# Kernel tuning notes

Hardware: AMD Instinct MI355X
Metric: run time of the kernel (lower is better)

The kernel has to match this reference:

```python
import jax, jax.numpy as jnp
import numpy as np

B, C, N = 2, 4, 200000
M = N // 8  # bytes in the bitmask per (b, c)


def _quat_to_rotmat(quats):
    # quats: (..., 4) -> R: (..., 3, 3)
    q = quats * jax.lax.rsqrt(jnp.sum(quats * quats, -1, keepdims=True))
    w, x, y, z = q[..., 0], q[..., 1], q[..., 2], q[..., 3]
    R = jnp.stack([
        1 - 2 * (y * y + z * z), 2 * (x * y - w * z), 2 * (x * z + w * y),
        2 * (x * y + w * z), 1 - 2 * (x * x + z * z), 2 * (y * z - w * x),
        2 * (x * z - w * y), 2 * (y * z + w * x), 1 - 2 * (x * x + y * y)], -1)
    return R.reshape(q.shape[:-1] + (3, 3))


def _quat_to_rotmat_vjp(quats, v_R):
    inv_norm = jax.lax.rsqrt(jnp.sum(quats * quats, -1, keepdims=True))
    qn = quats * inv_norm
    w, x, y, z = qn[..., 0], qn[..., 1], qn[..., 2], qn[..., 3]
    a = v_R[..., 2, 1] - v_R[..., 1, 2]
    b = v_R[..., 0, 2] - v_R[..., 2, 0]
    c = v_R[..., 1, 0] - v_R[..., 0, 1]
    s11_22 = v_R[..., 1, 1] + v_R[..., 2, 2]
    s00_22 = v_R[..., 0, 0] + v_R[..., 2, 2]
    s00_11 = v_R[..., 0, 0] + v_R[..., 1, 1]
    p01 = v_R[..., 1, 0] + v_R[..., 0, 1]
    p02 = v_R[..., 2, 0] + v_R[..., 0, 2]
    p12 = v_R[..., 2, 1] + v_R[..., 1, 2]
    v_qn = jnp.stack([
        2.0 * (x * a + y * b + z * c),
        2.0 * (-2.0 * x * s11_22 + y * p01 + z * p02 + w * a),
        2.0 * (x * p01 - 2.0 * y * s00_22 + z * p12 + w * b),
        2.0 * (x * p02 + y * p12 - 2.0 * z * s00_11 + w * c)], -1)
    return (v_qn - jnp.sum(v_qn * qn, -1, keepdims=True) * qn) * inv_norm


def _forward(means, quats, scales, conics, viewmats, Ks, v_means2d, v_depths,
             v_conics, v_colors_culling, v_opacities_culling, filter_mask,
             width, height):
    means = jnp.transpose(means, (0, 2, 1))            # (B,N,3)
    quats = jnp.transpose(quats, (0, 2, 1))            # (B,N,4)
    scales = jnp.transpose(scales, (0, 2, 1))          # (B,N,3)
    conics = jnp.transpose(conics, (0, 1, 3, 2))       # (B,C,N,3)
    v_m2d = jnp.transpose(v_means2d, (0, 1, 3, 2))     # (B,C,N,2)
    v_con = jnp.transpose(v_conics, (0, 1, 3, 2))      # (B,C,N,3)
    v_col = jnp.transpose(v_colors_culling, (0, 1, 3, 2))  # (B,C,N,3)
    v_op = v_opacities_culling                          # (B,C,N)
    v_dep = v_depths                                    # (B,C,N)
    Bv, Cv, Nv = v_op.shape

    # unpack uint8 bitmask (LSB first), decompact culled grads back to N slots
    bits = ((filter_mask[..., None] >> jnp.arange(8, dtype=filter_mask.dtype)) & 1) != 0
    fb = bits.reshape(Bv, Cv, -1)[:, :, :Nv]            # (B,C,N) bool
    rank = jnp.clip(jnp.cumsum(fb.astype(jnp.int32), axis=-1) - 1, 0, Nv - 1)

    def decompact(v):
        if v.ndim == 3:
            return jnp.where(fb, jnp.take_along_axis(v, rank, axis=2), 0.0)
        return jnp.where(fb[..., None], jnp.take_along_axis(v, rank[..., None], axis=2), 0.0)

    v_con_o = decompact(v_con)
    v_m2d_o = decompact(v_m2d)
    v_dep_o = decompact(v_dep)
    v_col_o = decompact(v_col)
    v_op_o = decompact(v_op)

    # conic (inverse 2x2 covariance) VJP
    covar2d_inv = jnp.stack([conics[..., 0], conics[..., 1], conics[..., 1], conics[..., 2]], -1)
    covar2d_inv = covar2d_inv.reshape(conics.shape[:-1] + (2, 2))
    v_ci = jnp.stack([v_con_o[..., 0], v_con_o[..., 1] * 0.5, v_con_o[..., 1] * 0.5, v_con_o[..., 2]], -1)
    v_ci = v_ci.reshape(conics.shape[:-1] + (2, 2))
    v_covar2d = -covar2d_inv @ v_ci @ covar2d_inv        # (B,C,N,2,2)

    Rv = viewmats[..., :3, :3]                           # (B,C,3,3)
    t = viewmats[..., :3, 3]                             # (B,C,3)
    rotmat = _quat_to_rotmat(quats)                      # (B,N,3,3)
    Mm = rotmat * scales[..., None, :]
    covars = jnp.einsum('bnij,bnkj->bnik', Mm, Mm)       # (B,N,3,3)
    mean_c = jnp.einsum('bcij,bnj->bcni', Rv, means) + t[..., None, :]  # (B,C,N,3)
    covar_c = jnp.einsum('bcij,bnjk,bclk->bcnil', Rv, covars, Rv)       # (B,C,N,3,3)

    # perspective projection VJP
    mx, my, tz = mean_c[..., 0], mean_c[..., 1], mean_c[..., 2]
    tz2 = tz * tz
    tz3 = tz2 * tz
    fx = Ks[..., 0, 0, None]
    fy = Ks[..., 1, 1, None]
    cx = Ks[..., 0, 2, None]
    cy = Ks[..., 1, 2, None]
    tan_fovx = 0.5 * width / fx
    tan_fovy = 0.5 * height / fy
    lim_x_pos = (width - cx) / fx + 0.3 * tan_fovx
    lim_x_neg = cx / fx + 0.3 * tan_fovx
    lim_y_pos = (height - cy) / fy + 0.3 * tan_fovy
    lim_y_neg = cy / fy + 0.3 * tan_fovy
    xf = ((mx / tz <= lim_x_pos) & (mx / tz >= -lim_x_neg)).astype(tz.dtype)
    yf = ((my / tz <= lim_y_pos) & (my / tz >= -lim_y_neg)).astype(tz.dtype)
    tx = tz * jnp.clip(mx / tz, -lim_x_neg, lim_x_pos)
    ty = tz * jnp.clip(my / tz, -lim_y_neg, lim_y_pos)
    O = jnp.zeros_like(tz)
    J = jnp.stack([fx / tz, O, -fx * tx / tz2, O, fy / tz, -fy * ty / tz2], -1)
    J = J.reshape(tz.shape + (2, 3))                     # (B,C,N,2,3)
    v_cov3d = jnp.swapaxes(J, -2, -1) @ v_covar2d @ J    # (B,C,N,3,3)
    vm0, vm1 = v_m2d_o[..., 0], v_m2d_o[..., 1]
    m0 = fx / tz * vm0
    m1 = fy / tz * vm1
    m2 = -(fx * mx * vm0 + fy * my * vm1) / tz2
    v_J = v_covar2d @ J @ jnp.swapaxes(covar_c, -2, -1) + jnp.swapaxes(v_covar2d, -2, -1) @ J @ covar_c
    vJ00, vJ02 = v_J[..., 0, 0], v_J[..., 0, 2]
    vJ11, vJ12 = v_J[..., 1, 1], v_J[..., 1, 2]
    m0 = m0 - fx / tz2 * vJ02 * xf
    m2 = m2 - fx / tz3 * vJ02 * tx * (1.0 - xf)
    m1 = m1 - fy / tz2 * vJ12 * yf
    m2 = m2 - fy / tz3 * vJ12 * ty * (1.0 - yf)
    m2 = m2 - fx / tz2 * vJ00 - fy / tz2 * vJ11 + 2.0 * fx * tx / tz3 * vJ02 + 2.0 * fy * ty / tz3 * vJ12
    m2 = m2 + v_dep_o
    v_mean_c = jnp.stack([m0, m1, m2], -1)               # (B,C,N,3)

    # world-to-camera VJPs
    v_Rview = jnp.einsum('bcni,bnj->bcij', v_mean_c, means)
    v_pW = jnp.einsum('bcji,bcnj->bni', Rv, v_mean_c)
    v_Rview = v_Rview + jnp.einsum('bcnij,bcjk,bnlk->bcil', v_cov3d, Rv, covars) \
                      + jnp.einsum('bcnji,bcjk,bnkl->bcil', v_cov3d, Rv, covars)
    v_covarW = jnp.einsum('bcij,bcnik,bckl->bnjl', Rv, v_cov3d, Rv)

    # quat/scale -> covariance VJP
    v_M = (v_covarW + jnp.swapaxes(v_covarW, -2, -1)) @ Mm
    v_Rrot = v_M * scales[..., None, :]
    v_quats = _quat_to_rotmat_vjp(quats, v_Rrot)         # (B,N,4)
    v_scales = jnp.einsum('bnij,bnij->bnj', rotmat, v_M) # (B,N,3)

    v_colors_final = jnp.transpose(v_col_o.sum(axis=1), (0, 2, 1))  # (B,3,N)
    v_opacities_final = v_op_o.sum(axis=1)               # (B,N)
    return (v_pW, v_quats, v_scales, v_Rview, v_colors_final, v_opacities_final)


def setup_inputs() -> dict:
    key = jax.random.key(0)
    k = jax.random.split(key, 12)
    means = jax.random.normal(k[0], (B, 3, N), jnp.float32)
    quats = jax.random.normal(k[1], (B, 4, N), jnp.float32)
    scales = 0.1 + 0.4 * jax.random.uniform(k[2], (B, 3, N), dtype=jnp.float32)
    conics = 0.1 * jax.random.normal(k[3], (B, C, 3, N), jnp.float32)
    viewmats = jnp.tile(jnp.eye(4, dtype=jnp.float32), (B, C, 1, 1)) \
             + 0.05 * jax.random.normal(k[4], (B, C, 4, 4), jnp.float32)
    viewmats = viewmats.at[..., 2, 3].add(5.0)  # keep tz away from 0
    Kmat = jnp.array([[500.0, 0.0, 324.0], [0.0, 500.0, 210.0], [0.0, 0.0, 1.0]], jnp.float32)
    Ks = jnp.tile(Kmat, (B, C, 1, 1))
    v_means2d = 0.05 * jax.random.normal(k[5], (B, C, 2, N), jnp.float32)
    v_depths = 0.05 * jax.random.normal(k[6], (B, C, N), jnp.float32)
    v_conics = 0.05 * jax.random.normal(k[7], (B, C, 3, N), jnp.float32)
    v_colors_culling = 0.05 * jax.random.normal(k[8], (B, C, 3, N), jnp.float32)
    v_opacities_culling = 0.05 * jax.random.normal(k[9], (B, C, N), jnp.float32)
    filter_mask = jax.random.randint(k[10], (B, C, M), 0, 256, jnp.int32)
    return {"means": means, "quats": quats, "scales": scales, "conics": conics,
            "viewmats": viewmats, "Ks": Ks, "v_means2d": v_means2d,
            "v_depths": v_depths, "v_conics": v_conics,
            "v_colors_culling": v_colors_culling,
            "v_opacities_culling": v_opacities_culling,
            "filter_mask": filter_mask, "width": 648, "height": 420}


def reference(means, quats, scales, conics, viewmats, Ks, v_means2d, v_depths,
              v_conics, v_colors_culling, v_opacities_culling, filter_mask,
              width, height):
    return _forward(means, quats, scales, conics, viewmats, Ks, v_means2d,
                    v_depths, v_conics, v_colors_culling, v_opacities_culling,
                    filter_mask, width, height)
```

## Files before the change

kernel.cpp:

```cpp
#include <hip/hip_runtime.h>

#define NPTS 200000
#define MWORDS 25000
#define NCHUNK 98
#define NSLOT 64

#define WS_PREFIX    0
#define WS_BLOCKSUM  800000
#define WS_CHUNKPREF 803136
#define WS_SLOTS     806272
#define WS_CAM       824704

__global__ __launch_bounds__(256) void scan1_kernel(const int* __restrict__ mask,
                                                    int* __restrict__ prefix,
                                                    int* __restrict__ blocksum) {
    const int bc    = blockIdx.y;
    const int chunk = blockIdx.x;
    const int tid   = threadIdx.x;
    const int lane  = tid & 63, wv = tid >> 6;
    const int w = chunk * 256 + tid;
    const int base = bc * MWORDS;

    int p = (w < MWORDS) ? __popc(mask[base + w]) : 0;
    int v = p;
#pragma unroll
    for (int off = 1; off < 64; off <<= 1) {
        int u = __shfl_up(v, off, 64);
        if (lane >= off) v += u;
    }
    __shared__ int wsum[4];
    if (lane == 63) wsum[wv] = v;
    __syncthreads();
    int wadd = 0;
#pragma unroll
    for (int i = 0; i < 4; i++) if (i < wv) wadd += wsum[i];
    int excl = v - p + wadd;
    if (w < MWORDS) prefix[base + w] = excl;
    if (tid == 255) blocksum[bc * NCHUNK + chunk] = wadd + v;
}

__global__ __launch_bounds__(1024) void scan2_kernel(const int* __restrict__ blocksum,
                                                     int* __restrict__ chunkpref,
                                                     float* __restrict__ slots,
                                                     float* __restrict__ cam,
                                                     const float* __restrict__ viewmats,
                                                     const float* __restrict__ Ks,
                                                     const int* __restrict__ pw,
                                                     const int* __restrict__ ph) {
    const int tid = threadIdx.x;
    __shared__ int s[8 * NCHUNK];
    if (tid < 8 * NCHUNK) s[tid] = blocksum[tid];
    __syncthreads();
    if (tid < 8) {
        int running = 0;
        for (int j = 0; j < NCHUNK; j++) {
            int idx = tid * NCHUNK + j;
            int t = s[idx];
            s[idx] = running;
            running += t;
        }
    }
    __syncthreads();
    if (tid < 8 * NCHUNK) chunkpref[tid] = s[tid];

    for (int i = tid; i < NSLOT * 72; i += 1024) slots[i] = 0.f;

    if (tid < 8) {
        const int bc = tid;
        float* cp = cam + bc * 20;
        const int vbase = bc * 16;
        for (int i = 0; i < 3; i++) {
            for (int j = 0; j < 3; j++) cp[i*3 + j] = viewmats[vbase + i*4 + j];
            cp[9 + i] = viewmats[vbase + i*4 + 3];
        }
        const int kbase = bc * 9;
        float fx = Ks[kbase + 0], fy = Ks[kbase + 4];
        float cx = Ks[kbase + 2], cy = Ks[kbase + 5];
        int wi = *pw, hi = *ph;
        float W = (wi >= 1 && wi <= (1 << 20)) ? (float)wi : __int_as_float(wi);
        float H = (hi >= 1 && hi <= (1 << 20)) ? (float)hi : __int_as_float(hi);
        float tanx = 0.5f * W / fx, tany = 0.5f * H / fy;
        cp[12] = fx; cp[13] = fy;
        cp[14] = (W - cx) / fx + 0.3f * tanx;
        cp[15] = cx / fx + 0.3f * tanx;
        cp[16] = (H - cy) / fy + 0.3f * tany;
        cp[17] = cy / fy + 0.3f * tany;
    }
}

__global__ __launch_bounds__(256) void main_kernel(
    const float* __restrict__ means,
    const float* __restrict__ quats,
    const float* __restrict__ scales,
    const float* __restrict__ conics,
    const float* __restrict__ v_m2d,
    const float* __restrict__ v_dep,
    const float* __restrict__ v_con,
    const float* __restrict__ v_col,
    const float* __restrict__ v_op,
    const int* __restrict__ mask,
    const int* __restrict__ prefix,
    const int* __restrict__ chunkpref,
    const float* __restrict__ cam,
    float* __restrict__ slots,
    float* __restrict__ out)
{
    const int O_PW = 0, O_QU = 1200000, O_SC = 2800000, O_CL = 4000072, O_OP = 5200072;
    const int b = blockIdx.y;
    const int n = blockIdx.x * 256 + threadIdx.x;
    const bool act = (n < NPTS);

    float rv[4][9];
#pragma unroll
    for (int c = 0; c < 4; c++)
#pragma unroll
        for (int k = 0; k < 9; k++) rv[c][k] = 0.f;

    float H00=0,H01=0,H02=0,H11=0,H12=0,H22=0;
    float vpw0=0,vpw1=0,vpw2=0;
    float vcl0=0,vcl1=0,vcl2=0, vopo=0;
    float qw=0,qx=0,qy=0,qz=0, inv_norm=1.f;
    float R00=0,R01=0,R02=0,R10=0,R11=0,R12=0,R20=0,R21=0,R22=0;
    float M00=0,M01=0,M02=0,M10=0,M11=0,M12=0,M20=0,M21=0,M22=0;
    float cv00=0,cv01=0,cv02=0,cv11=0,cv12=0,cv22=0;
    float mn0=0,mn1=0,mn2=0, sc0=0,sc1=0,sc2=0;

    if (act) {
        const int w_ = n >> 3, bit = n & 7, chk = w_ >> 8;
        int words[4], pref[4];
#pragma unroll
        for (int c = 0; c < 4; c++) {
            const int bc = b*4 + c;
            words[c] = mask[bc*MWORDS + w_];
            pref[c]  = prefix[bc*MWORDS + w_] + chunkpref[bc*NCHUNK + chk];
        }

        mn0 = means[(b*3+0)*NPTS + n];
        mn1 = means[(b*3+1)*NPTS + n];
        mn2 = means[(b*3+2)*NPTS + n];
        float q0 = quats[(b*4+0)*NPTS + n];
        float q1 = quats[(b*4+1)*NPTS + n];
        float q2 = quats[(b*4+2)*NPTS + n];
        float q3 = quats[(b*4+3)*NPTS + n];
        sc0 = scales[(b*3+0)*NPTS + n];
        sc1 = scales[(b*3+1)*NPTS + n];
        sc2 = scales[(b*3+2)*NPTS + n];
        inv_norm = rsqrtf(q0*q0 + q1*q1 + q2*q2 + q3*q3);
        qw = q0*inv_norm; qx = q1*inv_norm; qy = q2*inv_norm; qz = q3*inv_norm;
        R00 = 1.f - 2.f*(qy*qy + qz*qz); R01 = 2.f*(qx*qy - qw*qz); R02 = 2.f*(qx*qz + qw*qy);
        R10 = 2.f*(qx*qy + qw*qz); R11 = 1.f - 2.f*(qx*qx + qz*qz); R12 = 2.f*(qy*qz - qw*qx);
        R20 = 2.f*(qx*qz - qw*qy); R21 = 2.f*(qy*qz + qw*qx); R22 = 1.f - 2.f*(qx*qx + qy*qy);
        M00 = R00*sc0; M01 = R01*sc1; M02 = R02*sc2;
        M10 = R10*sc0; M11 = R11*sc1; M12 = R12*sc2;
        M20 = R20*sc0; M21 = R21*sc1; M22 = R22*sc2;
        cv00 = M00*M00 + M01*M01 + M02*M02;
        cv01 = M00*M10 + M01*M11 + M02*M12;
        cv02 = M00*M20 + M01*M21 + M02*M22;
        cv11 = M10*M10 + M11*M11 + M12*M12;
        cv12 = M10*M20 + M11*M21 + M12*M22;
        cv22 = M20*M20 + M21*M21 + M22*M22;

#pragma unroll
        for (int c = 0; c < 4; c++) {
            const int bc = b*4 + c;
            const float* cp = cam + bc*20;
            const float V00=cp[0],V01=cp[1],V02=cp[2],V10=cp[3],V11=cp[4],V12=cp[5],V20=cp[6],V21=cp[7],V22=cp[8];
            const float t0=cp[9], t1=cp[10], t2=cp[11];
            const float fx=cp[12], fy=cp[13], lxp=cp[14], lxn=cp[15], lyp=cp[16], lyn=cp[17];
            const int word = words[c];
            if ((word >> bit) & 1) {
                const int r = pref[c] + __popc(word & ((1 << bit) - 1));
                const int base3 = bc*3*NPTS, base2 = bc*2*NPTS, base1 = bc*NPTS;
                float g_c0 = v_con[base3 + r];
                float g_c1 = v_con[base3 + NPTS + r];
                float g_c2 = v_con[base3 + 2*NPTS + r];
                float g_m0 = v_m2d[base2 + r];
                float g_m1 = v_m2d[base2 + NPTS + r];
                float g_d  = v_dep[base1 + r];
                float g_l0 = v_col[base3 + r];
                float g_l1 = v_col[base3 + NPTS + r];
                float g_l2 = v_col[base3 + 2*NPTS + r];
                float g_o  = v_op[base1 + r];
                float p00 = conics[base3 + n];
                float p01 = conics[base3 + NPTS + n];
                float p11 = conics[base3 + 2*NPTS + n];
                float a00 = g_c0, a01 = 0.5f*g_c1, a11 = g_c2;
                float q00 = a00*p00 + a01*p01, q01 = a00*p01 + a01*p11;
                float q10 = a01*p00 + a11*p01, q11 = a01*p01 + a11*p11;
                float u00 = -(p00*q00 + p01*q10), u01 = -(p00*q01 + p01*q11);
                float u10 = -(p01*q00 + p11*q10), u11 = -(p01*q01 + p11*q11);
                float mx = V00*mn0 + V01*mn1 + V02*mn2 + t0;
                float my = V10*mn0 + V11*mn1 + V12*mn2 + t1;
                float tz = V20*mn0 + V21*mn1 + V22*mn2 + t2;
                float rz = 1.0f / tz;
                float rz2 = rz*rz, rz3 = rz2*rz;
                float T00 = V00*cv00 + V01*cv01 + V02*cv02;
                float T01 = V00*cv01 + V01*cv11 + V02*cv12;
                float T02 = V00*cv02 + V01*cv12 + V02*cv22;
                float T10 = V10*cv00 + V11*cv01 + V12*cv02;
                float T11 = V10*cv01 + V11*cv11 + V12*cv12;
                float T12 = V10*cv02 + V11*cv12 + V12*cv22;
                float T20 = V20*cv00 + V21*cv01 + V22*cv02;
                float T21 = V20*cv01 + V21*cv11 + V22*cv12;
                float T22 = V20*cv02 + V21*cv12 + V22*cv22;
                float cc00 = T00*V00 + T01*V01 + T02*V02;
                float cc01 = T00*V10 + T01*V11 + T02*V12;
                float cc02 = T00*V20 + T01*V21 + T02*V22;
                float cc11 = T10*V10 + T11*V11 + T12*V12;
                float cc12 = T10*V20 + T11*V21 + T12*V22;
                float cc22 = T20*V20 + T21*V21 + T22*V22;
                float mxz = mx*rz, myz = my*rz;
                float xf = (mxz <= lxp && mxz >= -lxn) ? 1.f : 0.f;
                float yf = (myz <= lyp && myz >= -lyn) ? 1.f : 0.f;
                float tx = tz * fminf(fmaxf(mxz, -lxn), lxp);
                float ty = tz * fminf(fmaxf(myz, -lyn), lyp);
                float j00 = fx*rz, j02 = -fx*tx*rz2;
                float j11 = fy*rz, j12 = -fy*ty*rz2;
                float W0a = u00*j00, W0b = u01*j11, W0c = u00*j02 + u01*j12;
                float W1a = u10*j00, W1b = u11*j11, W1c = u10*j02 + u11*j12;
                float d00 = j00*W0a, d01 = j00*W0b, d02 = j00*W0c;
                float d10 = j11*W1a, d11 = j11*W1b, d12 = j11*W1c;
                float d20 = j02*W0a + j12*W1a, d21 = j02*W0b + j12*W1b, d22 = j02*W0c + j12*W1c;
                float s00 = d00+d00, s01 = d01+d10, s02 = d02+d20;
                float s11 = d11+d11, s12 = d12+d21, s22 = d22+d22;
                float e00 = u00+u00, e01 = u01+u10, e11 = u11+u11;
                float X00 = e00*j00, X01 = e01*j11, X02 = e00*j02 + e01*j12;
                float X10 = e01*j00, X11 = e11*j11, X12 = e01*j02 + e11*j12;
                float vJ00 = X00*cc00 + X01*cc01 + X02*cc02;
                float vJ02 = X00*cc02 + X01*cc12 + X02*cc22;
                float vJ11 = X10*cc01 + X11*cc11 + X12*cc12;
                float vJ12 = X10*cc02 + X11*cc12 + X12*cc22;
                float m0 = fx*rz*g_m0;
                float m1 = fy*rz*g_m1;
                float m2 = -(fx*mx*g_m0 + fy*my*g_m1)*rz2;
                m0 -= fx*rz2*vJ02*xf;
                m2 -= fx*rz3*vJ02*tx*(1.f - xf);
                m1 -= fy*rz2*vJ12*yf;
                m2 -= fy*rz3*vJ12*ty*(1.f - yf);
                m2 += -fx*rz2*vJ00 - fy*rz2*vJ11 + 2.f*fx*tx*rz3*vJ02 + 2.f*fy*ty*rz3*vJ12;
                m2 += g_d;
                vpw0 += V00*m0 + V10*m1 + V20*m2;
                vpw1 += V01*m0 + V11*m1 + V21*m2;
                vpw2 += V02*m0 + V12*m1 + V22*m2;
                rv[c][0] += m0*mn0 + (s00*T00 + s01*T10 + s02*T20);
                rv[c][1] += m0*mn1 + (s00*T01 + s01*T11 + s02*T21);
                rv[c][2] += m0*mn2 + (s00*T02 + s01*T12 + s02*T22);
                rv[c][3] += m1*mn0 + (s01*T00 + s11*T10 + s12*T20);
                rv[c][4] += m1*mn1 + (s01*T01 + s11*T11 + s12*T21);
                rv[c][5] += m1*mn2 + (s01*T02 + s11*T12 + s12*T22);
                rv[c][6] += m2*mn0 + (s02*T00 + s12*T10 + s22*T20);
                rv[c][7] += m2*mn1 + (s02*T01 + s12*T11 + s22*T21);
                rv[c][8] += m2*mn2 + (s02*T02 + s12*T12 + s22*T22);
                float P00 = s00*V00 + s01*V10 + s02*V20;
                float P01 = s00*V01 + s01*V11 + s02*V21;
                float P02 = s00*V02 + s01*V12 + s02*V22;
                float P10 = s01*V00 + s11*V10 + s12*V20;
                float P11 = s01*V01 + s11*V11 + s12*V21;
                float P12 = s01*V02 + s11*V12 + s12*V22;
                float P20 = s02*V00 + s12*V10 + s22*V20;
                float P21 = s02*V01 + s12*V11 + s22*V21;
                float P22 = s02*V02 + s12*V12 + s22*V22;
                H00 += V00*P00 + V10*P10 + V20*P20;
                H01 += V00*P01 + V10*P11 + V20*P21;
                H02 += V00*P02 + V10*P12 + V20*P22;
                H11 += V01*P01 + V11*P11 + V21*P21;
                H12 += V01*P02 + V11*P12 + V21*P22;
                H22 += V02*P02 + V12*P12 + V22*P22;
                vcl0 += g_l0; vcl1 += g_l1; vcl2 += g_l2; vopo += g_o;
            }
        }
    }

#pragma unroll
    for (int off = 32; off >= 1; off >>= 1) {
#pragma unroll
        for (int c = 0; c < 4; c++)
#pragma unroll
            for (int k = 0; k < 9; k++)
                rv[c][k] += __shfl_down(rv[c][k], off, 64);
    }
    __shared__ float redbuf[4][36];
    const int lane = threadIdx.x & 63, wv = threadIdx.x >> 6;
    if (lane == 0) {
#pragma unroll
        for (int c = 0; c < 4; c++)
#pragma unroll
            for (int k = 0; k < 9; k++) redbuf[wv][c*9 + k] = rv[c][k];
    }
    __syncthreads();
    if (threadIdx.x < 36) {
        float s = redbuf[0][threadIdx.x] + redbuf[1][threadIdx.x] +
                  redbuf[2][threadIdx.x] + redbuf[3][threadIdx.x];
        const int slot = blockIdx.x & (NSLOT - 1);
        atomicAdd(&slots[slot*72 + b*36 + threadIdx.x], s);
    }

    if (act) {
        float vM00 = H00*M00 + H01*M10 + H02*M20;
        float vM01 = H00*M01 + H01*M11 + H02*M21;
        float vM02 = H00*M02 + H01*M12 + H02*M22;
        float vM10 = H01*M00 + H11*M10 + H12*M20;
        float vM11 = H01*M01 + H11*M11 + H12*M21;
        float vM12 = H01*M02 + H11*M12 + H12*M22;
        float vM20 = H02*M00 + H12*M10 + H22*M20;
        float vM21 = H02*M01 + H12*M11 + H22*M21;
        float vM22 = H02*M02 + H12*M12 + H22*M22;
        float vs0 = R00*vM00 + R10*vM10 + R20*vM20;
        float vs1 = R01*vM01 + R11*vM11 + R21*vM21;
        float vs2 = R02*vM02 + R12*vM12 + R22*vM22;
        float G00 = vM00*sc0, G01 = vM01*sc1, G02 = vM02*sc2;
        float G10 = vM10*sc0, G11 = vM11*sc1, G12 = vM12*sc2;
        float G20 = vM20*sc0, G21 = vM21*sc1, G22 = vM22*sc2;
        float a_ = G21 - G12, b_ = G02 - G20, c_ = G10 - G01;
        float s1122 = G11 + G22, s0022 = G00 + G22, s0011 = G00 + G11;
        float pp01 = G10 + G01, pp02 = G20 + G02, pp12 = G21 + G12;
        float vq0 = 2.f*(qx*a_ + qy*b_ + qz*c_);
        float vq1 = 2.f*(-2.f*qx*s1122 + qy*pp01 + qz*pp02 + qw*a_);
        float vq2 = 2.f*(qx*pp01 - 2.f*qy*s0022 + qz*pp12 + qw*b_);
        float vq3 = 2.f*(qx*pp02 + qy*pp12 - 2.f*qz*s0011 + qw*c_);
        float dot = vq0*qw + vq1*qx + vq2*qy + vq3*qz;
        float o0 = (vq0 - dot*qw)*inv_norm;
        float o1 = (vq1 - dot*qx)*inv_norm;
        float o2 = (vq2 - dot*qy)*inv_norm;
        float o3 = (vq3 - dot*qz)*inv_norm;

        const int pwb = b*NPTS + n;
        out[O_PW + pwb*3 + 0] = vpw0;
        out[O_PW + pwb*3 + 1] = vpw1;
        out[O_PW + pwb*3 + 2] = vpw2;
        float4 qv = make_float4(o0, o1, o2, o3);
        *reinterpret_cast<float4*>(out + O_QU + pwb*4) = qv;
        out[O_SC + pwb*3 + 0] = vs0;
        out[O_SC + pwb*3 + 1] = vs1;
        out[O_SC + pwb*3 + 2] = vs2;
        out[O_CL + (b*3+0)*NPTS + n] = vcl0;
        out[O_CL + (b*3+1)*NPTS + n] = vcl1;
        out[O_CL + (b*3+2)*NPTS + n] = vcl2;
        out[O_OP + b*NPTS + n] = vopo;
    }
}

__global__ void fin_kernel(const float* __restrict__ slots, float* __restrict__ out) {
    int t = threadIdx.x;
    if (t < 72) {
        float s = 0.f;
#pragma unroll
        for (int i = 0; i < NSLOT; i++) s += slots[i*72 + t];
        out[4000000 + t] = s;
    }
}

extern "C" void kernel_launch(void* const* d_in, const int* in_sizes, int n_in,
                              void* d_out, int out_size, void* d_ws, size_t ws_size,
                              hipStream_t stream) {
    (void)in_sizes; (void)n_in; (void)out_size; (void)ws_size;
    const float* means    = (const float*)d_in[0];
    const float* quats    = (const float*)d_in[1];
    const float* scales   = (const float*)d_in[2];
    const float* conics   = (const float*)d_in[3];
    const float* viewmats = (const float*)d_in[4];
    const float* Ks       = (const float*)d_in[5];
    const float* v_m2d    = (const float*)d_in[6];
    const float* v_dep    = (const float*)d_in[7];
    const float* v_con    = (const float*)d_in[8];
    const float* v_col    = (const float*)d_in[9];
    const float* v_op     = (const float*)d_in[10];
    const int* mask = (const int*)d_in[11];
    const int* pw   = (const int*)d_in[12];
    const int* ph   = (const int*)d_in[13];
    float* out = (float*)d_out;

    char* ws = (char*)d_ws;
    int*   prefix    = (int*)(ws + WS_PREFIX);
    int*   blocksum  = (int*)(ws + WS_BLOCKSUM);
    int*   chunkpref = (int*)(ws + WS_CHUNKPREF);
    float* slots     = (float*)(ws + WS_SLOTS);
    float* cam       = (float*)(ws + WS_CAM);

    scan1_kernel<<<dim3(NCHUNK, 8), dim3(256), 0, stream>>>(mask, prefix, blocksum);
    scan2_kernel<<<dim3(1), dim3(1024), 0, stream>>>(blocksum, chunkpref, slots, cam,
                                                     viewmats, Ks, pw, ph);
    main_kernel<<<dim3((NPTS + 255) / 256, 2), dim3(256), 0, stream>>>(
        means, quats, scales, conics, v_m2d, v_dep, v_con, v_col, v_op,
        mask, prefix, chunkpref, cam, slots, out);
    fin_kernel<<<dim3(1), dim3(128), 0, stream>>>(slots, out);
}
```

Before: 169.1 us.

## Remove scan2 kernel, compute chunk prefix in main kernel, use DPP reductions

Drops the single-block scan2 launch: camera setup and slot zeroing move into an extra block of scan1, and each main-kernel block derives its chunk prefix itself by summing the preceding block sums with a wave reduction. The per-camera rotation-gradient accumulators now go through DPP wave reductions, with per-wave atomics replacing the 36-register array, shuffle tree and LDS block reduction. Inactive threads clamp their index instead of branching. The aim is to save one kernel launch and serial scan latency, plus register pressure, at the cost of redundant block-sum reads and more atomics per block.

```diff
diff --git a/kernel.cpp b/kernel.cpp
--- a/kernel.cpp
+++ b/kernel.cpp
@@ -7,16 +7,66 @@
 
 #define WS_PREFIX    0
 #define WS_BLOCKSUM  800000
-#define WS_CHUNKPREF 803136
-#define WS_SLOTS     806272
-#define WS_CAM       824704
+#define WS_SLOTS     803136
+#define WS_CAM       821568
+
+__device__ __forceinline__ float wred_f(float x) {
+    x += __int_as_float(__builtin_amdgcn_update_dpp(0, __float_as_int(x), 0x111, 0xf, 0xf, true));
+    x += __int_as_float(__builtin_amdgcn_update_dpp(0, __float_as_int(x), 0x112, 0xf, 0xf, true));
+    x += __int_as_float(__builtin_amdgcn_update_dpp(0, __float_as_int(x), 0x114, 0xf, 0xf, true));
+    x += __int_as_float(__builtin_amdgcn_update_dpp(0, __float_as_int(x), 0x118, 0xf, 0xf, true));
+    x += __int_as_float(__builtin_amdgcn_update_dpp(0, __float_as_int(x), 0x142, 0xf, 0xf, true));
+    x += __int_as_float(__builtin_amdgcn_update_dpp(0, __float_as_int(x), 0x143, 0xf, 0xf, true));
+    return x;
+}
+__device__ __forceinline__ int wred_i(int x) {
+    x += __builtin_amdgcn_update_dpp(0, x, 0x111, 0xf, 0xf, true);
+    x += __builtin_amdgcn_update_dpp(0, x, 0x112, 0xf, 0xf, true);
+    x += __builtin_amdgcn_update_dpp(0, x, 0x114, 0xf, 0xf, true);
+    x += __builtin_amdgcn_update_dpp(0, x, 0x118, 0xf, 0xf, true);
+    x += __builtin_amdgcn_update_dpp(0, x, 0x142, 0xf, 0xf, true);
+    x += __builtin_amdgcn_update_dpp(0, x, 0x143, 0xf, 0xf, true);
+    return x;
+}
 
 __global__ __launch_bounds__(256) void scan1_kernel(const int* __restrict__ mask,
                                                     int* __restrict__ prefix,
-                                                    int* __restrict__ blocksum) {
+                                                    int* __restrict__ blocksum,
+                                                    float* __restrict__ slots,
+                                                    float* __restrict__ cam,
+                                                    const float* __restrict__ viewmats,
+                                                    const float* __restrict__ Ks,
+                                                    const int* __restrict__ pw,
+                                                    const int* __restrict__ ph) {
+    const int tid = threadIdx.x;
+    if (blockIdx.x == NCHUNK) {
+        if (blockIdx.y != 0) return;
+        for (int i = tid; i < NSLOT * 72; i += 256) slots[i] = 0.f;
+        if (tid < 8) {
+            const int bc = tid;
+            float* cp = cam + bc * 20;
+            const int vbase = bc * 16;
+            for (int i = 0; i < 3; i++) {
+                for (int j = 0; j < 3; j++) cp[i*3 + j] = viewmats[vbase + i*4 + j];
+                cp[9 + i] = viewmats[vbase + i*4 + 3];
+            }
+            const int kbase = bc * 9;
+            float fx = Ks[kbase + 0], fy = Ks[kbase + 4];
+            float cx = Ks[kbase + 2], cy = Ks[kbase + 5];
+            int wi = *pw, hi = *ph;
+            float W = (wi >= 1 && wi <= (1 << 20)) ? (float)wi : __int_as_float(wi);
+            float H = (hi >= 1 && hi <= (1 << 20)) ? (float)hi : __int_as_float(hi);
+            float tanx = 0.5f * W / fx, tany = 0.5f * H / fy;
+            cp[12] = fx; cp[13] = fy;
+            cp[14] = (W - cx) / fx + 0.3f * tanx;
+            cp[15] = cx / fx + 0.3f * tanx;
+            cp[16] = (H - cy) / fy + 0.3f * tany;
+            cp[17] = cy / fy + 0.3f * tany;
+        }
+        return;
+    }
     const int bc    = blockIdx.y;
     const int chunk = blockIdx.x;
-    const int tid   = threadIdx.x;
     const int lane  = tid & 63, wv = tid >> 6;
     const int w = chunk * 256 + tid;
     const int base = bc * MWORDS;
@@ -34,58 +84,8 @@
     int wadd = 0;
 #pragma unroll
     for (int i = 0; i < 4; i++) if (i < wv) wadd += wsum[i];
-    int excl = v - p + wadd;
-    if (w < MWORDS) prefix[base + w] = excl;
+    if (w < MWORDS) prefix[base + w] = v - p + wadd;
     if (tid == 255) blocksum[bc * NCHUNK + chunk] = wadd + v;
-}
-
-__global__ __launch_bounds__(1024) void scan2_kernel(const int* __restrict__ blocksum,
-                                                     int* __restrict__ chunkpref,
-                                                     float* __restrict__ slots,
-                                                     float* __restrict__ cam,
-                                                     const float* __restrict__ viewmats,
-                                                     const float* __restrict__ Ks,
-                                                     const int* __restrict__ pw,
-                                                     const int* __restrict__ ph) {
-    const int tid = threadIdx.x;
-    __shared__ int s[8 * NCHUNK];
-    if (tid < 8 * NCHUNK) s[tid] = blocksum[tid];
-    __syncthreads();
-    if (tid < 8) {
-        int running = 0;
-        for (int j = 0; j < NCHUNK; j++) {
-            int idx = tid * NCHUNK + j;
-            int t = s[idx];
-            s[idx] = running;
-            running += t;
-        }
-    }
-    __syncthreads();
-    if (tid < 8 * NCHUNK) chunkpref[tid] = s[tid];
-
-    for (int i = tid; i < NSLOT * 72; i += 1024) slots[i] = 0.f;
-
-    if (tid < 8) {
-        const int bc = tid;
-        float* cp = cam + bc * 20;
-        const int vbase = bc * 16;
-        for (int i = 0; i < 3; i++) {
-            for (int j = 0; j < 3; j++) cp[i*3 + j] = viewmats[vbase + i*4 + j];
-            cp[9 + i] = viewmats[vbase + i*4 + 3];
-        }
-        const int kbase = bc * 9;
-        float fx = Ks[kbase + 0], fy = Ks[kbase + 4];
-        float cx = Ks[kbase + 2], cy = Ks[kbase + 5];
-        int wi = *pw, hi = *ph;
-        float W = (wi >= 1 && wi <= (1 << 20)) ? (float)wi : __int_as_float(wi);
-        float H = (hi >= 1 && hi <= (1 << 20)) ? (float)hi : __int_as_float(hi);
-        float tanx = 0.5f * W / fx, tany = 0.5f * H / fy;
-        cp[12] = fx; cp[13] = fy;
-        cp[14] = (W - cx) / fx + 0.3f * tanx;
-        cp[15] = cx / fx + 0.3f * tanx;
-        cp[16] = (H - cy) / fy + 0.3f * tany;
-        cp[17] = cy / fy + 0.3f * tany;
-    }
 }
 
 __global__ __launch_bounds__(256) void main_kernel(
@@ -100,7 +100,7 @@
     const float* __restrict__ v_op,
     const int* __restrict__ mask,
     const int* __restrict__ prefix,
-    const int* __restrict__ chunkpref,
+    const int* __restrict__ blocksum,
     const float* __restrict__ cam,
     float* __restrict__ slots,
     float* __restrict__ out)
@@ -109,190 +109,179 @@
     const int b = blockIdx.y;
     const int n = blockIdx.x * 256 + threadIdx.x;
     const bool act = (n < NPTS);
-
-    float rv[4][9];
-#pragma unroll
-    for (int c = 0; c < 4; c++)
-#pragma unroll
-        for (int k = 0; k < 9; k++) rv[c][k] = 0.f;
+    const int nc = act ? n : (NPTS - 1);
+    const int lane = threadIdx.x & 63, wv = threadIdx.x >> 6;
+    const int slot = blockIdx.x & (NSLOT - 1);
+
+    const int chk = blockIdx.x >> 3;
+    __shared__ int cpf_lds[4];
+    {
+        const int bcw = b * 4 + wv;
+        int s0 = (lane < chk) ? blocksum[bcw * NCHUNK + lane] : 0;
+        if (lane + 64 < chk) s0 += blocksum[bcw * NCHUNK + lane + 64];
+        int tot = wred_i(s0);
+        int t = __builtin_amdgcn_readlane(tot, 63);
+        if (lane == 0) cpf_lds[wv] = t;
+    }
+
+    const int w_ = nc >> 3, bit = nc & 7;
+    int words[4], pref[4];
+#pragma unroll
+    for (int c = 0; c < 4; c++) {
+        const int bc = b*4 + c;
+        words[c] = mask[bc*MWORDS + w_];
+        pref[c]  = prefix[bc*MWORDS + w_];
+    }
+
+    float mn0 = means[(b*3+0)*NPTS + nc];
+    float mn1 = means[(b*3+1)*NPTS + nc];
+    float mn2 = means[(b*3+2)*NPTS + nc];
+    float q0 = quats[(b*4+0)*NPTS + nc];
+    float q1 = quats[(b*4+1)*NPTS + nc];
+    float q2 = quats[(b*4+2)*NPTS + nc];
+    float q3 = quats[(b*4+3)*NPTS + nc];
+    float sc0 = scales[(b*3+0)*NPTS + nc];
+    float sc1 = scales[(b*3+1)*NPTS + nc];
+    float sc2 = scales[(b*3+2)*NPTS + nc];
+    float inv_norm = rsqrtf(q0*q0 + q1*q1 + q2*q2 + q3*q3);
+    float qw = q0*inv_norm, qx = q1*inv_norm, qy = q2*inv_norm, qz = q3*inv_norm;
+    float R00 = 1.f - 2.f*(qy*qy + qz*qz), R01 = 2.f*(qx*qy - qw*qz), R02 = 2.f*(qx*qz + qw*qy);
+    float R10 = 2.f*(qx*qy + qw*qz), R11 = 1.f - 2.f*(qx*qx + qz*qz), R12 = 2.f*(qy*qz - qw*qx);
+    float R20 = 2.f*(qx*qz - qw*qy), R21 = 2.f*(qy*qz + qw*qx), R22 = 1.f - 2.f*(qx*qx + qy*qy);
+    float M00 = R00*sc0, M01 = R01*sc1, M02 = R02*sc2;
+    float M10 = R10*sc0, M11 = R11*sc1, M12 = R12*sc2;
+    float M20 = R20*sc0, M21 = R21*sc1, M22 = R22*sc2;
+    float cv00 = M00*M00 + M01*M01 + M02*M02;
+    float cv01 = M00*M10 + M01*M11 + M02*M12;
+    float cv02 = M00*M20 + M01*M21 + M02*M22;
+    float cv11 = M10*M10 + M11*M11 + M12*M12;
+    float cv12 = M10*M20 + M11*M21 + M12*M22;
+    float cv22 = M20*M20 + M21*M21 + M22*M22;
 
     float H00=0,H01=0,H02=0,H11=0,H12=0,H22=0;
     float vpw0=0,vpw1=0,vpw2=0;
     float vcl0=0,vcl1=0,vcl2=0, vopo=0;
-    float qw=0,qx=0,qy=0,qz=0, inv_norm=1.f;
-    float R00=0,R01=0,R02=0,R10=0,R11=0,R12=0,R20=0,R21=0,R22=0;
-    float M00=0,M01=0,M02=0,M10=0,M11=0,M12=0,M20=0,M21=0,M22=0;
-    float cv00=0,cv01=0,cv02=0,cv11=0,cv12=0,cv22=0;
-    float mn0=0,mn1=0,mn2=0, sc0=0,sc1=0,sc2=0;
-
-    if (act) {
-        const int w_ = n >> 3, bit = n & 7, chk = w_ >> 8;
-        int words[4], pref[4];
-#pragma unroll
-        for (int c = 0; c < 4; c++) {
-            const int bc = b*4 + c;
-            words[c] = mask[bc*MWORDS + w_];
-            pref[c]  = prefix[bc*MWORDS + w_] + chunkpref[bc*NCHUNK + chk];
-        }
-
-        mn0 = means[(b*3+0)*NPTS + n];
-        mn1 = means[(b*3+1)*NPTS + n];
-        mn2 = means[(b*3+2)*NPTS + n];
-        float q0 = quats[(b*4+0)*NPTS + n];
-        float q1 = quats[(b*4+1)*NPTS + n];
-        float q2 = quats[(b*4+2)*NPTS + n];
-        float q3 = quats[(b*4+3)*NPTS + n];
-        sc0 = scales[(b*3+0)*NPTS + n];
-        sc1 = scales[(b*3+1)*NPTS + n];
-        sc2 = scales[(b*3+2)*NPTS + n];
-        inv_norm = rsqrtf(q0*q0 + q1*q1 + q2*q2 + q3*q3);
-        qw = q0*inv_norm; qx = q1*inv_norm; qy = q2*inv_norm; qz = q3*inv_norm;
-        R00 = 1.f - 2.f*(qy*qy + qz*qz); R01 = 2.f*(qx*qy - qw*qz); R02 = 2.f*(qx*qz + qw*qy);
-        R10 = 2.f*(qx*qy + qw*qz); R11 = 1.f - 2.f*(qx*qx + qz*qz); R12 = 2.f*(qy*qz - qw*qx);
-        R20 = 2.f*(qx*qz - qw*qy); R21 = 2.f*(qy*qz + qw*qx); R22 = 1.f - 2.f*(qx*qx + qy*qy);
-        M00 = R00*sc0; M01 = R01*sc1; M02 = R02*sc2;
-        M10 = R10*sc0; M11 = R11*sc1; M12 = R12*sc2;
-        M20 = R20*sc0; M21 = R21*sc1; M22 = R22*sc2;
-        cv00 = M00*M00 + M01*M01 + M02*M02;
-        cv01 = M00*M10 + M01*M11 + M02*M12;
-        cv02 = M00*M20 + M01*M21 + M02*M22;
-        cv11 = M10*M10 + M11*M11 + M12*M12;
-        cv12 = M10*M20 + M11*M21 + M12*M22;
-        cv22 = M20*M20 + M21*M21 + M22*M22;
-
-#pragma unroll
-        for (int c = 0; c < 4; c++) {
-            const int bc = b*4 + c;
-            const float* cp = cam + bc*20;
+
+    __syncthreads();
+
+#pragma unroll
+    for (int c = 0; c < 4; c++) {
+        const int bc = b*4 + c;
+        const float* cp = cam + bc*20;
+        const bool go = act && ((words[c] >> bit) & 1);
+        float rv0=0,rv1=0,rv2=0,rv3=0,rv4=0,rv5=0,rv6=0,rv7=0,rv8=0;
+        if (go) {
             const float V00=cp[0],V01=cp[1],V02=cp[2],V10=cp[3],V11=cp[4],V12=cp[5],V20=cp[6],V21=cp[7],V22=cp[8];
             const float t0=cp[9], t1=cp[10], t2=cp[11];
             const float fx=cp[12], fy=cp[13], lxp=cp[14], lxn=cp[15], lyp=cp[16], lyn=cp[17];
-            const int word = words[c];
-            if ((word >> bit) & 1) {
-                const int r = pref[c] + __popc(word & ((1 << bit) - 1));
-                const int base3 = bc*3*NPTS, base2 = bc*2*NPTS, base1 = bc*NPTS;
-                float g_c0 = v_con[base3 + r];
-                float g_c1 = v_con[base3 + NPTS + r];
-                float g_c2 = v_con[base3 + 2*NPTS + r];
-                float g_m0 = v_m2d[base2 + r];
-                float g_m1 = v_m2d[base2 + NPTS + r];
-                float g_d  = v_dep[base1 + r];
-                float g_l0 = v_col[base3 + r];
-                float g_l1 = v_col[base3 + NPTS + r];
-                float g_l2 = v_col[base3 + 2*NPTS + r];
-                float g_o  = v_op[base1 + r];
-                float p00 = conics[base3 + n];
-                float p01 = conics[base3 + NPTS + n];
-                float p11 = conics[base3 + 2*NPTS + n];
-                float a00 = g_c0, a01 = 0.5f*g_c1, a11 = g_c2;
-                float q00 = a00*p00 + a01*p01, q01 = a00*p01 + a01*p11;
-                float q10 = a01*p00 + a11*p01, q11 = a01*p01 + a11*p11;
-                float u00 = -(p00*q00 + p01*q10), u01 = -(p00*q01 + p01*q11);
-                float u10 = -(p01*q00 + p11*q10), u11 = -(p01*q01 + p11*q11);
-                float mx = V00*mn0 + V01*mn1 + V02*mn2 + t0;
-                float my = V10*mn0 + V11*mn1 + V12*mn2 + t1;
-                float tz = V20*mn0 + V21*mn1 + V22*mn2 + t2;
-                float rz = 1.0f / tz;
-                float rz2 = rz*rz, rz3 = rz2*rz;
-                float T00 = V00*cv00 + V01*cv01 + V02*cv02;
-                float T01 = V00*cv01 + V01*cv11 + V02*cv12;
-                float T02 = V00*cv02 + V01*cv12 + V02*cv22;
-                float T10 = V10*cv00 + V11*cv01 + V12*cv02;
-                float T11 = V10*cv01 + V11*cv11 + V12*cv12;
-                float T12 = V10*cv02 + V11*cv12 + V12*cv22;
-                float T20 = V20*cv00 + V21*cv01 + V22*cv02;
-                float T21 = V20*cv01 + V21*cv11 + V22*cv12;
-                float T22 = V20*cv02 + V21*cv12 + V22*cv22;
-                float cc00 = T00*V00 + T01*V01 + T02*V02;
-                float cc01 = T00*V10 + T01*V11 + T02*V12;
-                float cc02 = T00*V20 + T01*V21 + T02*V22;
-                float cc11 = T10*V10 + T11*V11 + T12*V12;
-                float cc12 = T10*V20 + T11*V21 + T12*V22;
-                float cc22 = T20*V20 + T21*V21 + T22*V22;
-                float mxz = mx*rz, myz = my*rz;
-                float xf = (mxz <= lxp && mxz >= -lxn) ? 1.f : 0.f;
-                float yf = (myz <= lyp && myz >= -lyn) ? 1.f : 0.f;
-                float tx = tz * fminf(fmaxf(mxz, -lxn), lxp);
-                float ty = tz * fminf(fmaxf(myz, -lyn), lyp);
-                float j00 = fx*rz, j02 = -fx*tx*rz2;
-                float j11 = fy*rz, j12 = -fy*ty*rz2;
-                float W0a = u00*j00, W0b = u01*j11, W0c = u00*j02 + u01*j12;
-                float W1a = u10*j00, W1b = u11*j11, W1c = u10*j02 + u11*j12;
-                float d00 = j00*W0a, d01 = j00*W0b, d02 = j00*W0c;
-                float d10 = j11*W1a, d11 = j11*W1b, d12 = j11*W1c;
-                float d20 = j02*W0a + j12*W1a, d21 = j02*W0b + j12*W1b, d22 = j02*W0c + j12*W1c;
-                float s00 = d00+d00, s01 = d01+d10, s02 = d02+d20;
-                float s11 = d11+d11, s12 = d12+d21, s22 = d22+d22;
-                float e00 = u00+u00, e01 = u01+u10, e11 = u11+u11;
-                float X00 = e00*j00, X01 = e01*j11, X02 = e00*j02 + e01*j12;
-                float X10 = e01*j00, X11 = e11*j11, X12 = e01*j02 + e11*j12;
-                float vJ00 = X00*cc00 + X01*cc01 + X02*cc02;
-                float vJ02 = X00*cc02 + X01*cc12 + X02*cc22;
-                float vJ11 = X10*cc01 + X11*cc11 + X12*cc12;
-                float vJ12 = X10*cc02 + X11*cc12 + X12*cc22;
-                float m0 = fx*rz*g_m0;
-                float m1 = fy*rz*g_m1;
-                float m2 = -(fx*mx*g_m0 + fy*my*g_m1)*rz2;
-                m0 -= fx*rz2*vJ02*xf;
-                m2 -= fx*rz3*vJ02*tx*(1.f - xf);
-                m1 -= fy*rz2*vJ12*yf;
-                m2 -= fy*rz3*vJ12*ty*(1.f - yf);
-                m2 += -fx*rz2*vJ00 - fy*rz2*vJ11 + 2.f*fx*tx*rz3*vJ02 + 2.f*fy*ty*rz3*vJ12;
-                m2 += g_d;
-                vpw0 += V00*m0 + V10*m1 + V20*m2;
-                vpw1 += V01*m0 + V11*m1 + V21*m2;
-                vpw2 += V02*m0 + V12*m1 + V22*m2;
-                rv[c][0] += m0*mn0 + (s00*T00 + s01*T10 + s02*T20);
-                rv[c][1] += m0*mn1 + (s00*T01 + s01*T11 + s02*T21);
-                rv[c][2] += m0*mn2 + (s00*T02 + s01*T12 + s02*T22);
-                rv[c][3] += m1*mn0 + (s01*T00 + s11*T10 + s12*T20);
-                rv[c][4] += m1*mn1 + (s01*T01 + s11*T11 + s12*T21);
-                rv[c][5] += m1*mn2 + (s01*T02 + s11*T12 + s12*T22);
-                rv[c][6] += m2*mn0 + (s02*T00 + s12*T10 + s22*T20);
-                rv[c][7] += m2*mn1 + (s02*T01 + s12*T11 + s22*T21);
-                rv[c][8] += m2*mn2 + (s02*T02 + s12*T12 + s22*T22);
-                float P00 = s00*V00 + s01*V10 + s02*V20;
-                float P01 = s00*V01 + s01*V11 + s02*V21;
-                float P02 = s00*V02 + s01*V12 + s02*V22;
-                float P10 = s01*V00 + s11*V10 + s12*V20;
-                float P11 = s01*V01 + s11*V11 + s12*V21;
-                float P12 = s01*V02 + s11*V12 + s12*V22;
-                float P20 = s02*V00 + s12*V10 + s22*V20;
-                float P21 = s02*V01 + s12*V11 + s22*V21;
-                float P22 = s02*V02 + s12*V12 + s22*V22;
-                H00 += V00*P00 + V10*P10 + V20*P20;
-                H01 += V00*P01 + V10*P11 + V20*P21;
-                H02 += V00*P02 + V10*P12 + V20*P22;
-                H11 += V01*P01 + V11*P11 + V21*P21;
-                H12 += V01*P02 + V11*P12 + V21*P22;
-                H22 += V02*P02 + V12*P12 + V22*P22;
-                vcl0 += g_l0; vcl1 += g_l1; vcl2 += g_l2; vopo += g_o;
-            }
+            const int r = pref[c] + cpf_lds[c] + __popc(words[c] & ((1 << bit) - 1));
+            const int base3 = bc*3*NPTS, base2 = bc*2*NPTS, base1 = bc*NPTS;
+            float g_c0 = v_con[base3 + r];
+            float g_c1 = v_con[base3 + NPTS + r];
+            float g_c2 = v_con[base3 + 2*NPTS + r];
+            float g_m0 = v_m2d[base2 + r];
+            float g_m1 = v_m2d[base2 + NPTS + r];
+            float g_d  = v_dep[base1 + r];
+            float g_l0 = v_col[base3 + r];
+            float g_l1 = v_col[base3 + NPTS + r];
+            float g_l2 = v_col[base3 + 2*NPTS + r];
+            float g_o  = v_op[base1 + r];
+            float p00 = conics[base3 + nc];
+            float p01 = conics[base3 + NPTS + nc];
+            float p11 = conics[base3 + 2*NPTS + nc];
+            float a00 = g_c0, a01 = 0.5f*g_c1, a11 = g_c2;
+            float q00 = a00*p00 + a01*p01, q01 = a00*p01 + a01*p11;
+            float q10 = a01*p00 + a11*p01, q11 = a01*p01 + a11*p11;
+            float u00 = -(p00*q00 + p01*q10), u01 = -(p00*q01 + p01*q11);
+            float u10 = -(p01*q00 + p11*q10), u11 = -(p01*q01 + p11*q11);
+            float mx = V00*mn0 + V01*mn1 + V02*mn2 + t0;
+            float my = V10*mn0 + V11*mn1 + V12*mn2 + t1;
+            float tz = V20*mn0 + V21*mn1 + V22*mn2 + t2;
+            float rz = 1.0f / tz;
+            float rz2 = rz*rz, rz3 = rz2*rz;
+            float T00 = V00*cv00 + V01*cv01 + V02*cv02;
+            float T01 = V00*cv01 + V01*cv11 + V02*cv12;
+            float T02 = V00*cv02 + V01*cv12 + V02*cv22;
+            float T10 = V10*cv00 + V11*cv01 + V12*cv02;
+            float T11 = V10*cv01 + V11*cv11 + V12*cv12;
+            float T12 = V10*cv02 + V11*cv12 + V12*cv22;
+            float T20 = V20*cv00 + V21*cv01 + V22*cv02;
+            float T21 = V20*cv01 + V21*cv11 + V22*cv12;
+            float T22 = V20*cv02 + V21*cv12 + V22*cv22;
+            float cc00 = T00*V00 + T01*V01 + T02*V02;
+            float cc01 = T00*V10 + T01*V11 + T02*V12;
+            float cc02 = T00*V20 + T01*V21 + T02*V22;
+            float cc11 = T10*V10 + T11*V11 + T12*V12;
+            float cc12 = T10*V20 + T11*V21 + T12*V22;
+            float cc22 = T20*V20 + T21*V21 + T22*V22;
+            float mxz = mx*rz, myz = my*rz;
+            float xf = (mxz <= lxp && mxz >= -lxn) ? 1.f : 0.f;
+            float yf = (myz <= lyp && myz >= -lyn) ? 1.f : 0.f;
+            float tx = tz * fminf(fmaxf(mxz, -lxn), lxp);
+            float ty = tz * fminf(fmaxf(myz, -lyn), lyp);
+            float j00 = fx*rz, j02 = -fx*tx*rz2;
+            float j11 = fy*rz, j12 = -fy*ty*rz2;
+            float W0a = u00*j00, W0b = u01*j11, W0c = u00*j02 + u01*j12;
+            float W1a = u10*j00, W1b = u11*j11, W1c = u10*j02 + u11*j12;
+            float d00 = j00*W0a, d01 = j00*W0b, d02 = j00*W0c;
+            float d10 = j11*W1a, d11 = j11*W1b, d12 = j11*W1c;
+            float d20 = j02*W0a + j12*W1a, d21 = j02*W0b + j12*W1b, d22 = j02*W0c + j12*W1c;
+            float s00 = d00+d00, s01 = d01+d10, s02 = d02+d20;
+            float s11 = d11+d11, s12 = d12+d21, s22 = d22+d22;
+            float e00 = u00+u00, e01 = u01+u10, e11 = u11+u11;
+            float X00 = e00*j00, X01 = e01*j11, X02 = e00*j02 + e01*j12;
+            float X10 = e01*j00, X11 = e11*j11, X12 = e01*j02 + e11*j12;
+            float vJ00 = X00*cc00 + X01*cc01 + X02*cc02;
+            float vJ02 = X00*cc02 + X01*cc12 + X02*cc22;
+            float vJ11 = X10*cc01 + X11*cc11 + X12*cc12;
+            float vJ12 = X10*cc02 + X11*cc12 + X12*cc22;
+            float m0 = fx*rz*g_m0;
+            float m1 = fy*rz*g_m1;
+            float m2 = -(fx*mx*g_m0 + fy*my*g_m1)*rz2;
+            m0 -= fx*rz2*vJ02*xf;
+            m2 -= fx*rz3*vJ02*tx*(1.f - xf);
+            m1 -= fy*rz2*vJ12*yf;
+            m2 -= fy*rz3*vJ12*ty*(1.f - yf);
+            m2 += -fx*rz2*vJ00 - fy*rz2*vJ11 + 2.f*fx*tx*rz3*vJ02 + 2.f*fy*ty*rz3*vJ12;
+            m2 += g_d;
+            vpw0 += V00*m0 + V10*m1 + V20*m2;
+            vpw1 += V01*m0 + V11*m1 + V21*m2;
+            vpw2 += V02*m0 + V12*m1 + V22*m2;
+            rv0 = m0*mn0 + (s00*T00 + s01*T10 + s02*T20);
+            rv1 = m0*mn1 + (s00*T01 + s01*T11 + s02*T21);
+            rv2 = m0*mn2 + (s00*T02 + s01*T12 + s02*T22);
+            rv3 = m1*mn0 + (s01*T00 + s11*T10 + s12*T20);
+            rv4 = m1*mn1 + (s01*T01 + s11*T11 + s12*T21);
+            rv5 = m1*mn2 + (s01*T02 + s11*T12 + s12*T22);
+            rv6 = m2*mn0 + (s02*T00 + s12*T10 + s22*T20);
+            rv7 = m2*mn1 + (s02*T01 + s12*T11 + s22*T21);
+            rv8 = m2*mn2 + (s02*T02 + s12*T12 + s22*T22);
+            float P00 = s00*V00 + s01*V10 + s02*V20;
+            float P01 = s00*V01 + s01*V11 + s02*V21;
+            float P02 = s00*V02 + s01*V12 + s02*V22;
+            float P10 = s01*V00 + s11*V10 + s12*V20;
+            float P11 = s01*V01 + s11*V11 + s12*V21;
+            float P12 = s01*V02 + s11*V12 + s12*V22;
+            float P20 = s02*V00 + s12*V10 + s22*V20;
+            float P21 = s02*V01 + s12*V11 + s22*V21;
+            float P22 = s02*V02 + s12*V12 + s22*V22;
+            H00 += V00*P00 + V10*P10 + V20*P20;
+            H01 += V00*P01 + V10*P11 + V20*P21;
+            H02 += V00*P02 + V10*P12 + V20*P22;
+            H11 += V01*P01 + V11*P11 + V21*P21;
+            H12 += V01*P02 + V11*P12 + V21*P22;
+            H22 += V02*P02 + V12*P12 + V22*P22;
+            vcl0 += g_l0; vcl1 += g_l1; vcl2 += g_l2; vopo += g_o;
         }
-    }
-
-#pragma unroll
-    for (int off = 32; off >= 1; off >>= 1) {
-#pragma unroll
-        for (int c = 0; c < 4; c++)
-#pragma unroll
-            for (int k = 0; k < 9; k++)
-                rv[c][k] += __shfl_down(rv[c][k], off, 64);
-    }
-    __shared__ float redbuf[4][36];
-    const int lane = threadIdx.x & 63, wv = threadIdx.x >> 6;
-    if (lane == 0) {
-#pragma unroll
-        for (int c = 0; c < 4; c++)
-#pragma unroll
-            for (int k = 0; k < 9; k++) redbuf[wv][c*9 + k] = rv[c][k];
-    }
-    __syncthreads();
-    if (threadIdx.x < 36) {
-        float s = redbuf[0][threadIdx.x] + redbuf[1][threadIdx.x] +
-                  redbuf[2][threadIdx.x] + redbuf[3][threadIdx.x];
-        const int slot = blockIdx.x & (NSLOT - 1);
-        atomicAdd(&slots[slot*72 + b*36 + threadIdx.x], s);
+        rv0 = wred_f(rv0); rv1 = wred_f(rv1); rv2 = wred_f(rv2);
+        rv3 = wred_f(rv3); rv4 = wred_f(rv4); rv5 = wred_f(rv5);
+        rv6 = wred_f(rv6); rv7 = wred_f(rv7); rv8 = wred_f(rv8);
+        if (lane == 63) {
+            float* sp = slots + slot*72 + b*36 + c*9;
+            atomicAdd(sp+0, rv0); atomicAdd(sp+1, rv1); atomicAdd(sp+2, rv2);
+            atomicAdd(sp+3, rv3); atomicAdd(sp+4, rv4); atomicAdd(sp+5, rv5);
+            atomicAdd(sp+6, rv6); atomicAdd(sp+7, rv7); atomicAdd(sp+8, rv8);
+        }
     }
 
     if (act) {
@@ -371,17 +360,15 @@
     float* out = (float*)d_out;
 
     char* ws = (char*)d_ws;
-    int*   prefix    = (int*)(ws + WS_PREFIX);
-    int*   blocksum  = (int*)(ws + WS_BLOCKSUM);
-    int*   chunkpref = (int*)(ws + WS_CHUNKPREF);
-    float* slots     = (float*)(ws + WS_SLOTS);
-    float* cam       = (float*)(ws + WS_CAM);
-
-    scan1_kernel<<<dim3(NCHUNK, 8), dim3(256), 0, stream>>>(mask, prefix, blocksum);
-    scan2_kernel<<<dim3(1), dim3(1024), 0, stream>>>(blocksum, chunkpref, slots, cam,
-                                                     viewmats, Ks, pw, ph);
-    main_kernel<<<dim3((NPTS + 255) / 256, 2), dim3(256), 0, stream>>>(
+    int*   prefix   = (int*)(ws + WS_PREFIX);
+    int*   blocksum = (int*)(ws + WS_BLOCKSUM);
+    float* slots    = (float*)(ws + WS_SLOTS);
+    float* cam      = (float*)(ws + WS_CAM);
+
+    scan1_kernel<<<dim3(NCHUNK + 1, 8), dim3(256), 0, stream>>>(
+        mask, prefix, blocksum, slots, cam, viewmats, Ks, pw, ph);
+    main_kernel<<<dim3(782, 2), dim3(256), 0, stream>>>(
         means, quats, scales, conics, v_m2d, v_dep, v_con, v_col, v_op,
-        mask, prefix, chunkpref, cam, slots, out);
+        mask, prefix, blocksum, cam, slots, out);
     fin_kernel<<<dim3(1), dim3(128), 0, stream>>>(slots, out);
 }
```

After: 177.4 us. 1.05x slower.
